# Kernel tuning notes

Hardware: AMD Instinct MI355X
Metric: run time of the kernel (lower is better)

## Reference

```python
import jax, jax.numpy as jnp
import numpy as np

B = 4096
IN = 1024   # complex input size (real tensor width = 2*IN)
H = 1024    # complex hidden size
G = 4       # gates: f, i, a, o


def _cproj(xr, xi, Wr, Wi, br, bi):
    # Complex linear over a stacked gate axis.
    # xr, xi: [B, D]; Wr, Wi: [G, H, D]; br, bi: [G, H] -> ([B,G,H], [B,G,H])
    zr = jnp.einsum('bd,god->bgo', xr, Wr) - jnp.einsum('bd,god->bgo', xi, Wi) + br
    zi = jnp.einsum('bd,god->bgo', xr, Wi) + jnp.einsum('bd,god->bgo', xi, Wr) + bi
    return zr, zi


def _ctimes(ar, ai, br, bi):
    # complex elementwise multiply (a_r + i a_i) * (b_r + i b_i)
    return ar * br - ai * bi, ar * bi + ai * br


def setup_inputs() -> dict:
    key = jax.random.key(0)
    ks = jax.random.split(key, 11)
    s_in = 1.0 / np.sqrt(2 * IN)
    s_h = 1.0 / np.sqrt(2 * H)
    return {
        'input': jax.random.normal(ks[0], (B, 2 * IN), jnp.float32),
        'h_x': jax.random.normal(ks[1], (B, 2 * H), jnp.float32),
        'c_x': jax.random.normal(ks[2], (B, 2 * H), jnp.float32),
        # input-side CLinear weights stacked over gates [f, i, a, o]
        'Uw_r': jax.random.normal(ks[3], (G, H, IN), jnp.float32) * s_in,
        'Uw_i': jax.random.normal(ks[4], (G, H, IN), jnp.float32) * s_in,
        'Ub_r': jax.random.normal(ks[5], (G, H), jnp.float32) * s_in,
        'Ub_i': jax.random.normal(ks[6], (G, H), jnp.float32) * s_in,
        # hidden-side CLinear weights stacked over gates [f, i, a, o]
        'Ww_r': jax.random.normal(ks[7], (G, H, H), jnp.float32) * s_h,
        'Ww_i': jax.random.normal(ks[8], (G, H, H), jnp.float32) * s_h,
        'Wb_r': jax.random.normal(ks[9], (G, H), jnp.float32) * s_h,
        'Wb_i': jax.random.normal(ks[10], (G, H), jnp.float32) * s_h,
    }


def reference(input, h_x, c_x, Uw_r, Uw_i, Ub_r, Ub_i, Ww_r, Ww_i, Wb_r, Wb_i):
    xr, xi = input[:, :IN], input[:, IN:]
    hr, hi = h_x[:, :H], h_x[:, H:]
    cr, ci = c_x[:, :H], c_x[:, H:]

    # fused gate projections: z = W(h) + U(x), complex-valued, [B, 4, H]
    zu_r, zu_i = _cproj(xr, xi, Uw_r, Uw_i, Ub_r, Ub_i)
    zh_r, zh_i = _cproj(hr, hi, Ww_r, Ww_i, Wb_r, Wb_i)
    zr = zu_r + zh_r
    zi = zu_i + zh_i

    # gate activations (applied elementwise to real and imag halves alike)
    fr, fi = jax.nn.sigmoid(zr[:, 0]), jax.nn.sigmoid(zi[:, 0])
    ir, ii = jax.nn.sigmoid(zr[:, 1]), jax.nn.sigmoid(zi[:, 1])
    ar, ai = jnp.tanh(zr[:, 2]), jnp.tanh(zi[:, 2])
    orr, oi = jax.nn.sigmoid(zr[:, 3]), jax.nn.sigmoid(zi[:, 3])

    cf_r, cf_i = _ctimes(cr, ci, fr, fi)
    ai_r, ai_i = _ctimes(ar, ai, ir, ii)
    ct_r, ct_i = cf_r + ai_r, cf_i + ai_i

    ht_r, ht_i = _ctimes(orr, oi, jnp.tanh(ct_r), jnp.tanh(ct_i))

    h_t = jnp.concatenate((ht_r, ht_i), axis=1)
    c_t = jnp.concatenate((ct_r, ct_i), axis=1)
    return h_t, c_t
```

## Files before the change

### kernel.cpp

```cpp
#include <hip/hip_runtime.h>
#include <cstddef>


typedef short bf16x8 __attribute__((ext_vector_type(8)));
typedef float f32x4  __attribute__((ext_vector_type(4)));
typedef unsigned int u32x4 __attribute__((ext_vector_type(4)));

static constexpr int KDIM = 4096;
static constexpr size_t HOFF = (size_t)4096 * 2048;

__device__ __forceinline__ unsigned short f2bf(float f) {
    unsigned u = __float_as_uint(f);
    u += 0x7FFF + ((u >> 16) & 1);
    return (unsigned short)(u >> 16);
}

__device__ __forceinline__ u32x4 pack8(float4 a, float4 b) {
    u32x4 v;
    v.x = (unsigned)f2bf(a.x) | ((unsigned)f2bf(a.y) << 16);
    v.y = (unsigned)f2bf(a.z) | ((unsigned)f2bf(a.w) << 16);
    v.z = (unsigned)f2bf(b.x) | ((unsigned)f2bf(b.y) << 16);
    v.w = (unsigned)f2bf(b.z) | ((unsigned)f2bf(b.w) << 16);
    return v;
}

__device__ __forceinline__ float4 neg4(float4 v) {
    return make_float4(-v.x, -v.y, -v.z, -v.w);
}

__device__ __forceinline__ void async16(const void* g, void* l) {
    __builtin_amdgcn_global_load_lds(
        (const __attribute__((address_space(1))) unsigned int*)g,
        (__attribute__((address_space(3))) unsigned int*)l,
        16, 0, 0);
}

__device__ __forceinline__ float sigm(float x) { return 1.0f / (1.0f + __expf(-x)); }
__device__ __forceinline__ float tanh_(float x) {
    float e = __expf(2.0f * x);
    return (e - 1.0f) / (e + 1.0f);
}

__global__ __launch_bounds__(256) void pack_all(
    const float* __restrict__ input, const float* __restrict__ hx,
    const float* __restrict__ Uw_r, const float* __restrict__ Uw_i,
    const float* __restrict__ Ww_r, const float* __restrict__ Ww_i,
    const float* __restrict__ Ub_r, const float* __restrict__ Ub_i,
    const float* __restrict__ Wb_r, const float* __restrict__ Wb_i,
    unsigned short* __restrict__ Xb, unsigned short* __restrict__ Wb16,
    float* __restrict__ biasp) {
    int bid = blockIdx.x;
    if (bid < 4096) {
        int idx = bid * 256 + threadIdx.x;
        int r    = idx >> 8;
        int gcol = (idx & 255) * 16;
        const float* src = (gcol < 2048) ? (input + (size_t)r * 2048 + gcol)
                                         : (hx    + (size_t)r * 2048 + (gcol - 2048));
        float4 f0 = *(const float4*)src;
        float4 f1 = *(const float4*)(src + 4);
        float4 f2 = *(const float4*)(src + 8);
        float4 f3 = *(const float4*)(src + 12);
        *(u32x4*)(Xb + (size_t)idx * 16)     = pack8(f0, f1);
        *(u32x4*)(Xb + (size_t)idx * 16 + 8) = pack8(f2, f3);
    } else {
        int idx = (bid - 4096) * 256 + threadIdx.x;
        int np = idx >> 8;
        int k  = (idx & 255) * 16;
        int o = np >> 2, g = np & 3;
        int q = k >> 10, d = k & 1023;
        size_t sidx = (size_t)g * (1024 * 1024) + (size_t)o * 1024 + d;
        const float* srcR = (q < 2 ? Uw_r : Ww_r) + sidx;
        const float* srcI = (q < 2 ? Uw_i : Ww_i) + sidx;
        float4 r0 = *(const float4*)srcR;        float4 r1 = *(const float4*)(srcR + 4);
        float4 r2 = *(const float4*)(srcR + 8);  float4 r3 = *(const float4*)(srcR + 12);
        float4 i0 = *(const float4*)srcI;        float4 i1 = *(const float4*)(srcI + 4);
        float4 i2 = *(const float4*)(srcI + 8);  float4 i3 = *(const float4*)(srcI + 12);
        int n0 = o * 8 + g * 2;
        u32x4 p00, p01, p10, p11;
        if (q & 1) {
            p00 = pack8(neg4(i0), neg4(i1)); p01 = pack8(neg4(i2), neg4(i3));
            p10 = pack8(r0, r1);             p11 = pack8(r2, r3);
        } else {
            p00 = pack8(r0, r1);             p01 = pack8(r2, r3);
            p10 = pack8(i0, i1);             p11 = pack8(i2, i3);
        }
        *(u32x4*)(Wb16 + (size_t)n0 * KDIM + k)           = p00;
        *(u32x4*)(Wb16 + (size_t)n0 * KDIM + k + 8)       = p01;
        *(u32x4*)(Wb16 + (size_t)(n0 + 1) * KDIM + k)     = p10;
        *(u32x4*)(Wb16 + (size_t)(n0 + 1) * KDIM + k + 8) = p11;
        if (k == 0) {
            size_t bi = (size_t)g * 1024 + o;
            biasp[n0]     = Ub_r[bi] + Wb_r[bi];
            biasp[n0 + 1] = Ub_i[bi] + Wb_i[bi];
        }
    }
}

__global__ __launch_bounds__(512) void clstm_gemm(
    const unsigned short* __restrict__ Xb,
    const unsigned short* __restrict__ Wb,
    const float* __restrict__ biasp,
    const float* __restrict__ c_x,
    float* __restrict__ out) {
    extern __shared__ char smem[];

    const int tid  = threadIdx.x;
    const int lane = tid & 63;
    const int wave = tid >> 6;
    const int wm = wave >> 2, wn = wave & 3;
    const int quad = lane >> 4, col16 = lane & 15;

    const int bid = blockIdx.x;
    const int swz = (bid & 7) * 64 + (bid >> 3);
    const int st = swz >> 5, wi = swz & 31;
    const int mtile = (st & 3) * 4 + (wi & 3);
    const int ntile = (st >> 2) * 8 + (wi >> 2);

    const int srow  = tid >> 3;
    const int sslot = tid & 7;
    const unsigned short* pa[4];
    const unsigned short* pb[4];
#pragma unroll
    for (int i = 0; i < 4; ++i) {
        const int rowA = i * 64 + srow;
        const int c = sslot ^ (rowA & 7);
        pa[i] = Xb + (size_t)(mtile * 256 + rowA) * KDIM + c * 8;
        pb[i] = Wb + (size_t)(ntile * 256 + rowA) * KDIM + c * 8;
    }

    f32x4 acc[8][4] = {};

#pragma unroll
    for (int i = 0; i < 4; ++i) {
        async16(pa[i], smem + i * 8192 + wave * 1024);
        async16(pb[i], smem + 32768 + i * 8192 + wave * 1024);
        pa[i] += 64; pb[i] += 64;
    }

    const int rA0 = wm * 128 + col16;
    const int rB0 = wn * 64 + col16;

#pragma unroll 2
    for (int kt = 0; kt < 64; ++kt) {
        char* sA  = smem + (kt & 1) * 65536;
        char* sB  = sA + 32768;
        char* sAn = smem + (((kt & 1) ^ 1)) * 65536;
        char* sBn = sAn + 32768;

        __builtin_amdgcn_s_barrier();
        if (kt < 63) {
#pragma unroll
            for (int i = 0; i < 4; ++i) {
                async16(pa[i], sAn + i * 8192 + wave * 1024);
                async16(pb[i], sBn + i * 8192 + wave * 1024);
                pa[i] += 64; pb[i] += 64;
            }
            asm volatile("s_waitcnt vmcnt(8)" ::: "memory");
        } else {
            asm volatile("s_waitcnt vmcnt(0)" ::: "memory");
        }
        __builtin_amdgcn_s_barrier();

        bf16x8 bfr[4][2];
#pragma unroll
        for (int n = 0; n < 4; ++n)
#pragma unroll
            for (int ks = 0; ks < 2; ++ks) {
                const int r = rB0 + n * 16;
                const int ch = (ks * 4 + quad) ^ (r & 7);
                bfr[n][ks] = *(const bf16x8*)(sB + r * 128 + ch * 16);
            }
        bf16x8 af[2][2][2];
#pragma unroll
        for (int f = 0; f < 2; ++f)
#pragma unroll
            for (int ks = 0; ks < 2; ++ks) {
                const int r = rA0 + f * 16;
                const int ch = (ks * 4 + quad) ^ (r & 7);
                af[0][f][ks] = *(const bf16x8*)(sA + r * 128 + ch * 16);
            }

#pragma unroll
        for (int p = 0; p < 4; ++p) {
            const int cur = p & 1, nxt = cur ^ 1;
            if (p < 3) {
#pragma unroll
                for (int f = 0; f < 2; ++f)
#pragma unroll
                    for (int ks = 0; ks < 2; ++ks) {
                        const int r = rA0 + (p + 1) * 32 + f * 16;
                        const int ch = (ks * 4 + quad) ^ (r & 7);
                        af[nxt][f][ks] = *(const bf16x8*)(sA + r * 128 + ch * 16);
                    }
            }
            __builtin_amdgcn_s_setprio(1);
#pragma unroll
            for (int f = 0; f < 2; ++f)
#pragma unroll
                for (int n = 0; n < 4; ++n) {
                    acc[p * 2 + f][n] = __builtin_amdgcn_mfma_f32_16x16x32_bf16(
                        af[cur][f][0], bfr[n][0], acc[p * 2 + f][n], 0, 0, 0);
                    acc[p * 2 + f][n] = __builtin_amdgcn_mfma_f32_16x16x32_bf16(
                        af[cur][f][1], bfr[n][1], acc[p * 2 + f][n], 0, 0, 0);
                }
            __builtin_amdgcn_s_setprio(0);
        }
    }

    __syncthreads();
    float* zs = (float*)(smem + wave * 8192);
    const float* bp = biasp + ntile * 256 + wn * 64;
    const int o_idx = lane & 3;
    const int rgrp  = lane >> 2;

#pragma unroll
    for (int pass = 0; pass < 8; ++pass) {
        const int seg = pass >> 1;
        const int h   = pass & 1;
#pragma unroll
        for (int mf2 = 0; mf2 < 2; ++mf2)
#pragma unroll
            for (int tl = 0; tl < 2; ++tl) {
                int nf = h * 2 + tl;
                int colz = tl * 16 + col16;
#pragma unroll
                for (int r = 0; r < 4; ++r)
                    zs[(mf2 * 16 + quad * 4 + r) * 40 + colz] = acc[seg * 2 + mf2][nf][r];
            }

        float4 bb0 = *(const float4*)(bp + h * 32 + o_idx * 8);
        float4 bb1 = *(const float4*)(bp + h * 32 + o_idx * 8 + 4);
        int o_glob = ntile * 32 + wn * 8 + h * 4 + o_idx;

#pragma unroll
        for (int t = 0; t < 2; ++t) {
            int rowz = rgrp + t * 16;
            const float* zp = zs + rowz * 40 + o_idx * 8;
            float4 z0 = *(const float4*)zp;
            float4 z1 = *(const float4*)(zp + 4);
            int b = mtile * 256 + wm * 128 + seg * 32 + rowz;

            float fr = sigm(z0.x + bb0.x), fi = sigm(z0.y + bb0.y);
            float ir = sigm(z0.z + bb0.z), ii = sigm(z0.w + bb0.w);
            float ar = tanh_(z1.x + bb1.x), ai = tanh_(z1.y + bb1.y);
            float og_r = sigm(z1.z + bb1.z), og_i = sigm(z1.w + bb1.w);

            float cr = c_x[(size_t)b * 2048 + o_glob];
            float ci = c_x[(size_t)b * 2048 + 1024 + o_glob];

            float ct_r = (cr * fr - ci * fi) + (ar * ir - ai * ii);
            float ct_i = (cr * fi + ci * fr) + (ar * ii + ai * ir);
            float tr = tanh_(ct_r), ti = tanh_(ct_i);
            float ht_r = og_r * tr - og_i * ti;
            float ht_i = og_r * ti + og_i * tr;

            out[(size_t)b * 2048 + o_glob]               = ht_r;
            out[(size_t)b * 2048 + 1024 + o_glob]        = ht_i;
            out[HOFF + (size_t)b * 2048 + o_glob]        = ct_r;
            out[HOFF + (size_t)b * 2048 + 1024 + o_glob] = ct_i;
        }
        if (pass < 7)
            asm volatile("s_waitcnt lgkmcnt(0)" ::: "memory");
    }
}

extern "C" void kernel_launch(void* const* d_in, const int* in_sizes, int n_in,
                              void* d_out, int out_size, void* d_ws, size_t ws_size,
                              hipStream_t stream) {
    const float* input = (const float*)d_in[0];
    const float* h_x   = (const float*)d_in[1];
    const float* c_x   = (const float*)d_in[2];
    const float* Uw_r  = (const float*)d_in[3];
    const float* Uw_i  = (const float*)d_in[4];
    const float* Ub_r  = (const float*)d_in[5];
    const float* Ub_i  = (const float*)d_in[6];
    const float* Ww_r  = (const float*)d_in[7];
    const float* Ww_i  = (const float*)d_in[8];
    const float* Wb_r  = (const float*)d_in[9];
    const float* Wb_i  = (const float*)d_in[10];
    float* out = (float*)d_out;

    unsigned short* Xb   = (unsigned short*)d_ws;
    unsigned short* Wb16 = Xb + (size_t)4096 * 4096;
    float* biasp = (float*)(Wb16 + (size_t)8192 * 4096);

    static bool s_attr = false;
    if (!s_attr) {
        hipFuncSetAttribute((const void*)clstm_gemm,
                            hipFuncAttributeMaxDynamicSharedMemorySize, 131072);
        s_attr = true;
    }

    pack_all<<<8192, 256, 0, stream>>>(input, h_x, Uw_r, Uw_i, Ww_r, Ww_i,
                                       Ub_r, Ub_i, Wb_r, Wb_i, Xb, Wb16, biasp);
    clstm_gemm<<<512, 512, 131072, stream>>>(Xb, Wb16, biasp, c_x, out);
}
```

Baseline: 442.1 us.

## Interleave next-tile async loads with MFMA phases and drop one barrier

The K-loop used two barriers per iteration. Between them it issued all global-to-LDS async copies for the next tile and waited for the current tile. Now each iteration waits for all outstanding copies and uses a single barrier, then spreads the next tile's async copies across the first three MFMA phases. The second half of the B-fragment LDS reads is also deferred into phase 0, so the first MFMAs can start earlier. The aim is to cut barrier stalls and overlap memory issue with matrix math. The trade-off is a stricter vmcnt(0) wait and more scheduling complexity.

```diff
diff --git a/kernel.cpp b/kernel.cpp
--- a/kernel.cpp
+++ b/kernel.cpp
@@ -147,23 +147,12 @@
         char* sAn = smem + (((kt & 1) ^ 1)) * 65536;
         char* sBn = sAn + 32768;
 
+        asm volatile("s_waitcnt vmcnt(0)" ::: "memory");
         __builtin_amdgcn_s_barrier();
-        if (kt < 63) {
-#pragma unroll
-            for (int i = 0; i < 4; ++i) {
-                async16(pa[i], sAn + i * 8192 + wave * 1024);
-                async16(pb[i], sBn + i * 8192 + wave * 1024);
-                pa[i] += 64; pb[i] += 64;
-            }
-            asm volatile("s_waitcnt vmcnt(8)" ::: "memory");
-        } else {
-            asm volatile("s_waitcnt vmcnt(0)" ::: "memory");
-        }
-        __builtin_amdgcn_s_barrier();
 
         bf16x8 bfr[4][2];
 #pragma unroll
-        for (int n = 0; n < 4; ++n)
+        for (int n = 0; n < 2; ++n)
 #pragma unroll
             for (int ks = 0; ks < 2; ++ks) {
                 const int r = rB0 + n * 16;
@@ -183,6 +172,16 @@
 #pragma unroll
         for (int p = 0; p < 4; ++p) {
             const int cur = p & 1, nxt = cur ^ 1;
+            if (p == 0) {
+#pragma unroll
+                for (int n = 2; n < 4; ++n)
+#pragma unroll
+                    for (int ks = 0; ks < 2; ++ks) {
+                        const int r = rB0 + n * 16;
+                        const int ch = (ks * 4 + quad) ^ (r & 7);
+                        bfr[n][ks] = *(const bf16x8*)(sB + r * 128 + ch * 16);
+                    }
+            }
             if (p < 3) {
 #pragma unroll
                 for (int f = 0; f < 2; ++f)
@@ -193,16 +192,51 @@
                         af[nxt][f][ks] = *(const bf16x8*)(sA + r * 128 + ch * 16);
                     }
             }
+            if (kt < 63) {
+                if (p == 0) {
+                    async16(pa[0], sAn + 0 * 8192 + wave * 1024); pa[0] += 64;
+                    async16(pb[0], sBn + 0 * 8192 + wave * 1024); pb[0] += 64;
+                    async16(pa[1], sAn + 1 * 8192 + wave * 1024); pa[1] += 64;
+                    async16(pb[1], sBn + 1 * 8192 + wave * 1024); pb[1] += 64;
+                } else if (p == 1) {
+                    async16(pa[2], sAn + 2 * 8192 + wave * 1024); pa[2] += 64;
+                    async16(pb[2], sBn + 2 * 8192 + wave * 1024); pb[2] += 64;
+                } else if (p == 2) {
+                    async16(pa[3], sAn + 3 * 8192 + wave * 1024); pa[3] += 64;
+                    async16(pb[3], sBn + 3 * 8192 + wave * 1024); pb[3] += 64;
+                }
+            }
             __builtin_amdgcn_s_setprio(1);
-#pragma unroll
-            for (int f = 0; f < 2; ++f)
-#pragma unroll
-                for (int n = 0; n < 4; ++n) {
-                    acc[p * 2 + f][n] = __builtin_amdgcn_mfma_f32_16x16x32_bf16(
-                        af[cur][f][0], bfr[n][0], acc[p * 2 + f][n], 0, 0, 0);
-                    acc[p * 2 + f][n] = __builtin_amdgcn_mfma_f32_16x16x32_bf16(
-                        af[cur][f][1], bfr[n][1], acc[p * 2 + f][n], 0, 0, 0);
-                }
+            if (p == 0) {
+#pragma unroll
+                for (int f = 0; f < 2; ++f)
+#pragma unroll
+                    for (int n = 0; n < 2; ++n) {
+                        acc[f][n] = __builtin_amdgcn_mfma_f32_16x16x32_bf16(
+                            af[0][f][0], bfr[n][0], acc[f][n], 0, 0, 0);
+                        acc[f][n] = __builtin_amdgcn_mfma_f32_16x16x32_bf16(
+                            af[0][f][1], bfr[n][1], acc[f][n], 0, 0, 0);
+                    }
+#pragma unroll
+                for (int f = 0; f < 2; ++f)
+#pragma unroll
+                    for (int n = 2; n < 4; ++n) {
+                        acc[f][n] = __builtin_amdgcn_mfma_f32_16x16x32_bf16(
+                            af[0][f][0], bfr[n][0], acc[f][n], 0, 0, 0);
+                        acc[f][n] = __builtin_amdgcn_mfma_f32_16x16x32_bf16(
+                            af[0][f][1], bfr[n][1], acc[f][n], 0, 0, 0);
+                    }
+            } else {
+#pragma unroll
+                for (int f = 0; f < 2; ++f)
+#pragma unroll
+                    for (int n = 0; n < 4; ++n) {
+                        acc[p * 2 + f][n] = __builtin_amdgcn_mfma_f32_16x16x32_bf16(
+                            af[cur][f][0], bfr[n][0], acc[p * 2 + f][n], 0, 0, 0);
+                        acc[p * 2 + f][n] = __builtin_amdgcn_mfma_f32_16x16x32_bf16(
+                            af[cur][f][1], bfr[n][1], acc[p * 2 + f][n], 0, 0, 0);
+                    }
+            }
             __builtin_amdgcn_s_setprio(0);
         }
     }
```

After: 435.9 us. About the same (-1.4%).

## Switch to 32x32x16 MFMA and interleave async prefetch with compute phases

Applied to the files above, without the earlier changes.

Replaces the 16x16x32 bf16 MFMA tiling with 32x32x16 MFMAs, using f32x16 accumulators and precomputed swizzled LDS base offsets. Global-to-LDS async prefetches for the next k-tile are now spread across the four compute phases instead of issued in one burst before a second barrier. A full vmcnt(0) wait replaces the partial wait. The intent is fewer MFMA instructions and LDS reads per tile and better overlap of loads with math. The cost is a stricter wait at the top of each iteration and a remapped epilogue that must match the new accumulator layout.

```diff
diff --git a/kernel.cpp b/kernel.cpp
--- a/kernel.cpp
+++ b/kernel.cpp
@@ -3,7 +3,7 @@
 
 
 typedef short bf16x8 __attribute__((ext_vector_type(8)));
-typedef float f32x4  __attribute__((ext_vector_type(4)));
+typedef float f32x16 __attribute__((ext_vector_type(16)));
 typedef unsigned int u32x4 __attribute__((ext_vector_type(4)));
 
 static constexpr int KDIM = 4096;
@@ -108,7 +108,9 @@
     const int lane = tid & 63;
     const int wave = tid >> 6;
     const int wm = wave >> 2, wn = wave & 3;
-    const int quad = lane >> 4, col16 = lane & 15;
+    const int hi  = lane >> 5;
+    const int lo5 = lane & 31;
+    const int l7  = lane & 7;
 
     const int bid = blockIdx.x;
     const int swz = (bid & 7) * 64 + (bid >> 3);
@@ -128,7 +130,14 @@
         pb[i] = Wb + (size_t)(ntile * 256 + rowA) * KDIM + c * 8;
     }
 
-    f32x4 acc[8][4] = {};
+    int baseA[4], baseB[4];
+#pragma unroll
+    for (int s = 0; s < 4; ++s) {
+        baseA[s] = (wm * 128 + lo5) * 128 + (((s * 2 + hi) ^ l7) * 16);
+        baseB[s] = 32768 + (wn * 64 + lo5) * 128 + (((s * 2 + hi) ^ l7) * 16);
+    }
+
+    f32x16 acc[8] = {};
 
 #pragma unroll
     for (int i = 0; i < 4; ++i) {
@@ -137,72 +146,56 @@
         pa[i] += 64; pb[i] += 64;
     }
 
-    const int rA0 = wm * 128 + col16;
-    const int rB0 = wn * 64 + col16;
-
 #pragma unroll 2
     for (int kt = 0; kt < 64; ++kt) {
-        char* sA  = smem + (kt & 1) * 65536;
-        char* sB  = sA + 32768;
-        char* sAn = smem + (((kt & 1) ^ 1)) * 65536;
-        char* sBn = sAn + 32768;
-
+        const int bo  = (kt & 1) ? 65536 : 0;
+        const int bon = bo ^ 65536;
+        char* sAn = smem + bon;
+        char* sBn = smem + bon + 32768;
+
+        asm volatile("s_waitcnt vmcnt(0)" ::: "memory");
         __builtin_amdgcn_s_barrier();
-        if (kt < 63) {
-#pragma unroll
-            for (int i = 0; i < 4; ++i) {
-                async16(pa[i], sAn + i * 8192 + wave * 1024);
-                async16(pb[i], sBn + i * 8192 + wave * 1024);
-                pa[i] += 64; pb[i] += 64;
-            }
-            asm volatile("s_waitcnt vmcnt(8)" ::: "memory");
-        } else {
-            asm volatile("s_waitcnt vmcnt(0)" ::: "memory");
-        }
-        __builtin_amdgcn_s_barrier();
-
-        bf16x8 bfr[4][2];
-#pragma unroll
-        for (int n = 0; n < 4; ++n)
-#pragma unroll
-            for (int ks = 0; ks < 2; ++ks) {
-                const int r = rB0 + n * 16;
-                const int ch = (ks * 4 + quad) ^ (r & 7);
-                bfr[n][ks] = *(const bf16x8*)(sB + r * 128 + ch * 16);
-            }
-        bf16x8 af[2][2][2];
-#pragma unroll
-        for (int f = 0; f < 2; ++f)
-#pragma unroll
-            for (int ks = 0; ks < 2; ++ks) {
-                const int r = rA0 + f * 16;
-                const int ch = (ks * 4 + quad) ^ (r & 7);
-                af[0][f][ks] = *(const bf16x8*)(sA + r * 128 + ch * 16);
-            }
+
+        bf16x8 af[2][4], bf[2][2];
+#pragma unroll
+        for (int mb = 0; mb < 4; ++mb)
+            af[0][mb] = *(const bf16x8*)(smem + bo + baseA[0] + mb * 4096);
+#pragma unroll
+        for (int nb = 0; nb < 2; ++nb)
+            bf[0][nb] = *(const bf16x8*)(smem + bo + baseB[0] + nb * 4096);
 
 #pragma unroll
         for (int p = 0; p < 4; ++p) {
             const int cur = p & 1, nxt = cur ^ 1;
             if (p < 3) {
 #pragma unroll
-                for (int f = 0; f < 2; ++f)
-#pragma unroll
-                    for (int ks = 0; ks < 2; ++ks) {
-                        const int r = rA0 + (p + 1) * 32 + f * 16;
-                        const int ch = (ks * 4 + quad) ^ (r & 7);
-                        af[nxt][f][ks] = *(const bf16x8*)(sA + r * 128 + ch * 16);
-                    }
+                for (int mb = 0; mb < 4; ++mb)
+                    af[nxt][mb] = *(const bf16x8*)(smem + bo + baseA[p + 1] + mb * 4096);
+#pragma unroll
+                for (int nb = 0; nb < 2; ++nb)
+                    bf[nxt][nb] = *(const bf16x8*)(smem + bo + baseB[p + 1] + nb * 4096);
+            }
+            if (kt < 63) {
+                if (p == 0) {
+                    async16(pa[0], sAn + 0 * 8192 + wave * 1024); pa[0] += 64;
+                    async16(pb[0], sBn + 0 * 8192 + wave * 1024); pb[0] += 64;
+                    async16(pa[1], sAn + 1 * 8192 + wave * 1024); pa[1] += 64;
+                    async16(pb[1], sBn + 1 * 8192 + wave * 1024); pb[1] += 64;
+                } else if (p == 1) {
+                    async16(pa[2], sAn + 2 * 8192 + wave * 1024); pa[2] += 64;
+                    async16(pb[2], sBn + 2 * 8192 + wave * 1024); pb[2] += 64;
+                } else if (p == 2) {
+                    async16(pa[3], sAn + 3 * 8192 + wave * 1024); pa[3] += 64;
+                    async16(pb[3], sBn + 3 * 8192 + wave * 1024); pb[3] += 64;
+                }
             }
             __builtin_amdgcn_s_setprio(1);
 #pragma unroll
-            for (int f = 0; f < 2; ++f)
-#pragma unroll
-                for (int n = 0; n < 4; ++n) {
-                    acc[p * 2 + f][n] = __builtin_amdgcn_mfma_f32_16x16x32_bf16(
-                        af[cur][f][0], bfr[n][0], acc[p * 2 + f][n], 0, 0, 0);
-                    acc[p * 2 + f][n] = __builtin_amdgcn_mfma_f32_16x16x32_bf16(
-                        af[cur][f][1], bfr[n][1], acc[p * 2 + f][n], 0, 0, 0);
-                }
+            for (int mb = 0; mb < 4; ++mb)
+#pragma unroll
+                for (int nb = 0; nb < 2; ++nb)
+                    acc[mb * 2 + nb] = __builtin_amdgcn_mfma_f32_32x32x16_bf16(
+                        af[cur][mb], bf[cur][nb], acc[mb * 2 + nb], 0, 0, 0);
             __builtin_amdgcn_s_setprio(0);
         }
     }
@@ -215,22 +208,17 @@
 
 #pragma unroll
     for (int pass = 0; pass < 8; ++pass) {
-        const int seg = pass >> 1;
-        const int h   = pass & 1;
-#pragma unroll
-        for (int mf2 = 0; mf2 < 2; ++mf2)
-#pragma unroll
-            for (int tl = 0; tl < 2; ++tl) {
-                int nf = h * 2 + tl;
-                int colz = tl * 16 + col16;
-#pragma unroll
-                for (int r = 0; r < 4; ++r)
-                    zs[(mf2 * 16 + quad * 4 + r) * 40 + colz] = acc[seg * 2 + mf2][nf][r];
-            }
-
-        float4 bb0 = *(const float4*)(bp + h * 32 + o_idx * 8);
-        float4 bb1 = *(const float4*)(bp + h * 32 + o_idx * 8 + 4);
-        int o_glob = ntile * 32 + wn * 8 + h * 4 + o_idx;
+        const int mb = pass >> 1;
+        const int nb = pass & 1;
+#pragma unroll
+        for (int q = 0; q < 4; ++q)
+#pragma unroll
+            for (int j = 0; j < 4; ++j)
+                zs[(4 * hi + 8 * q + j) * 40 + lo5] = acc[mb * 2 + nb][q * 4 + j];
+
+        float4 bb0 = *(const float4*)(bp + nb * 32 + o_idx * 8);
+        float4 bb1 = *(const float4*)(bp + nb * 32 + o_idx * 8 + 4);
+        int o_glob = ntile * 32 + wn * 8 + nb * 4 + o_idx;
 
 #pragma unroll
         for (int t = 0; t < 2; ++t) {
@@ -238,7 +226,7 @@
             const float* zp = zs + rowz * 40 + o_idx * 8;
             float4 z0 = *(const float4*)zp;
             float4 z1 = *(const float4*)(zp + 4);
-            int b = mtile * 256 + wm * 128 + seg * 32 + rowz;
+            int b = mtile * 256 + wm * 128 + mb * 32 + rowz;
 
             float fr = sigm(z0.x + bb0.x), fi = sigm(z0.y + bb0.y);
             float ir = sigm(z0.z + bb0.z), ii = sigm(z0.w + bb0.w);
```

Result: slower. 464.1 us (+5.0%).
